# Kernel optimization log

Measured on AMD Instinct MI355X. Metric: run time of the kernel, lower is better.

The kernel has to match this reference:

```python
import jax, jax.numpy as jnp
import numpy as np

N = 10000      # nodes
E = 100000     # edges
D = 64         # node_out_feats
EH = 128       # edge_hidden_feats
NI = 74        # node_in_feats
EI = 12        # edge_in_feats
STEPS = 6


def _lin_init(key, fan_in, fan_out):
    s = 1.0 / np.sqrt(fan_in)
    kw, kb = jax.random.split(key)
    W = jax.random.uniform(kw, (fan_out, fan_in), minval=-s, maxval=s, dtype=jnp.float32)
    b = jax.random.uniform(kb, (fan_out,), minval=-s, maxval=s, dtype=jnp.float32)
    return W, b


def setup_inputs() -> dict:
    key = jax.random.key(0)
    ks = jax.random.split(key, 10)
    x = jax.random.normal(ks[0], (N, NI), dtype=jnp.float32)
    edge_index = jax.random.randint(ks[1], (2, E), 0, N, dtype=jnp.int64)
    edge_attr = jax.random.normal(ks[2], (E, EI), dtype=jnp.float32)
    W_proj, b_proj = _lin_init(ks[3], NI, D)
    W_e1, b_e1 = _lin_init(ks[4], EI, EH)
    W_e2, b_e2 = _lin_init(ks[5], EH, D * D)
    W_lin, b_lin = _lin_init(ks[6], D, D)
    s = 1.0 / np.sqrt(D)
    W_ih = jax.random.uniform(ks[7], (3 * D, D), minval=-s, maxval=s, dtype=jnp.float32)
    W_hh = jax.random.uniform(ks[8], (3 * D, D), minval=-s, maxval=s, dtype=jnp.float32)
    kb1, kb2 = jax.random.split(ks[9])
    b_ih = jax.random.uniform(kb1, (3 * D,), minval=-s, maxval=s, dtype=jnp.float32)
    b_hh = jax.random.uniform(kb2, (3 * D,), minval=-s, maxval=s, dtype=jnp.float32)
    return {"x": x, "edge_index": edge_index, "edge_attr": edge_attr,
            "W_proj": W_proj, "b_proj": b_proj,
            "W_e1": W_e1, "b_e1": b_e1, "W_e2": W_e2, "b_e2": b_e2,
            "W_lin": W_lin, "b_lin": b_lin,
            "W_ih": W_ih, "W_hh": W_hh, "b_ih": b_ih, "b_hh": b_hh}


def _gru_cell(x, h, W_ih, W_hh, b_ih, b_hh):
    # torch GRU gate layout: rows [r; z; n]
    gi = x @ W_ih.T + b_ih
    gh = h @ W_hh.T + b_hh
    i_r, i_z, i_n = jnp.split(gi, 3, axis=-1)
    h_r, h_z, h_n = jnp.split(gh, 3, axis=-1)
    r = jax.nn.sigmoid(i_r + h_r)
    z = jax.nn.sigmoid(i_z + h_z)
    n = jnp.tanh(i_n + r * h_n)
    return (1.0 - z) * n + z * h


def reference(x, edge_index, edge_attr, W_proj, b_proj, W_e1, b_e1, W_e2, b_e2,
              W_lin, b_lin, W_ih, W_hh, b_ih, b_hh):
    src = edge_index[0]
    dst = edge_index[1]
    n_nodes = x.shape[0]
    d = W_lin.shape[0]

    # project_node_feats
    node_feats = jax.nn.relu(x @ W_proj.T + b_proj)          # [N, D]
    hidden = node_feats                                       # h0 (never updated, per source)

    # edge network (identical each step in original; compute once)
    eh = jax.nn.relu(edge_attr @ W_e1.T + b_e1)               # [E, EH]
    A = (eh @ W_e2.T + b_e2).reshape(-1, d, d)                # [E, D, D]

    cnt = jax.ops.segment_sum(jnp.ones(src.shape, x.dtype), dst, num_segments=n_nodes)
    cnt = jnp.maximum(cnt, 1.0)[:, None]                      # mean divisor, 0-deg -> keep 0

    for _ in range(STEPS):
        xp = node_feats @ W_lin.T + b_lin                     # lin_node, [N, D]
        msg = jnp.einsum('ed,edf->ef', xp[src], A)            # per-edge bmm, [E, D]
        agg = jax.ops.segment_sum(msg, dst, num_segments=n_nodes) / cnt  # scatter-mean
        nf = jax.nn.relu(agg)
        node_feats = _gru_cell(nf, hidden, W_ih, W_hh, b_ih, b_hh)
    return node_feats
```

## Files before the change

### kernel.cpp

```cpp
#include <hip/hip_runtime.h>
#include <hip/hip_bf16.h>

#define NN 10000
#define NE 100000
#define DD 64
#define EH_ 128
#define NI_ 74
#define EI_ 12
#define NSTEPS 6
#define PADN 10240
#define GCAP 16384
#define EPB 64

#define RZ_OFF 0
#define NI_OFF 16384
#define NH_OFF 20480
#define WL_OFF 24576
#define BE_OFF 28672
#define G_TOT  32768

typedef short bf16x8 __attribute__((ext_vector_type(8)));
typedef float f32x4 __attribute__((ext_vector_type(4)));

static __device__ __forceinline__ unsigned short f2b(float f) {
    unsigned int u = __float_as_uint(f);
    u += 0x7fffu + ((u >> 16) & 1u);
    return (unsigned short)(u >> 16);
}

__global__ void k_zero(float* p, int n) {
    int i = blockIdx.x * blockDim.x + threadIdx.x;
    if (i < n) p[i] = 0.f;
}

__global__ void k_zero2(float* a, float* b, int n) {
    int i = blockIdx.x * blockDim.x + threadIdx.x;
    if (i < n) { a[i] = 0.f; b[i] = 0.f; }
}

__global__ void k_proj(const float* __restrict__ x, const float* __restrict__ Wp,
                       const float* __restrict__ bp, float* __restrict__ nf,
                       float* __restrict__ hid, unsigned short* __restrict__ hidb) {
    int w = (blockIdx.x * blockDim.x + threadIdx.x) >> 6;
    int lane = threadIdx.x & 63;
    if (w >= PADN) return;
    if (w >= NN) { hidb[(size_t)w * DD + lane] = 0; return; }
    const float* xr = x + (size_t)w * NI_;
    float x0 = xr[lane];
    float x1 = (lane < NI_ - 64) ? xr[64 + lane] : 0.f;
    float acc = bp[lane];
    const float* wr = Wp + (size_t)lane * NI_;
    #pragma unroll
    for (int i = 0; i < 64; i++) acc += __shfl(x0, i, 64) * wr[i];
    #pragma unroll
    for (int i = 0; i < NI_ - 64; i++) acc += __shfl(x1, i, 64) * wr[64 + i];
    acc = fmaxf(acc, 0.f);
    nf[(size_t)w * DD + lane] = acc;
    hid[(size_t)w * DD + lane] = acc;
    hidb[(size_t)w * DD + lane] = f2b(acc);
}

__global__ void k_degs(const int* __restrict__ srcv, const int* __restrict__ dstv,
                       int* __restrict__ hist, float* __restrict__ cnt) {
    int e = blockIdx.x * blockDim.x + threadIdx.x;
    if (e < NE) {
        atomicAdd(&hist[srcv[e]], 1);
        atomicAdd(&cnt[dstv[e]], 1.0f);
    }
}

__global__ void k_scangrp(const int* __restrict__ hist, int* __restrict__ rowptr,
                          int* __restrict__ cursor, int* __restrict__ g_src,
                          int* __restrict__ g_base, int* __restrict__ g_cnt,
                          int* __restrict__ d_ng) {
    __shared__ int part[1024];
    int t = threadIdx.x;
    const int PER = (NN + 1023) / 1024;
    int b0 = t * PER;
    int sum = 0;
    for (int i = 0; i < PER; i++) { int b = b0 + i; if (b < NN) sum += hist[b]; }
    part[t] = sum;
    __syncthreads();
    for (int off = 1; off < 1024; off <<= 1) {
        int v = (t >= off) ? part[t - off] : 0;
        __syncthreads();
        part[t] += v;
        __syncthreads();
    }
    int run = (t > 0) ? part[t - 1] : 0;
    for (int i = 0; i <= PER; i++) {
        int b = b0 + i;
        if (b <= NN) {
            rowptr[b] = run;
            if (b < NN) cursor[b] = run;
        }
        if (b < NN && i < PER) run += hist[b];
        if (i == PER) break;
    }
    __syncthreads();
    int cg = 0;
    for (int i = 0; i < PER; i++) {
        int b = b0 + i;
        if (b < NN) cg += (hist[b] + 15) >> 4;
    }
    part[t] = cg;
    __syncthreads();
    for (int off = 1; off < 1024; off <<= 1) {
        int v = (t >= off) ? part[t - off] : 0;
        __syncthreads();
        part[t] += v;
        __syncthreads();
    }
    int grun = (t > 0) ? part[t - 1] : 0;
    for (int i = 0; i < PER; i++) {
        int b = b0 + i;
        if (b >= NN) break;
        int r0 = rowptr[b], r1 = rowptr[b + 1];
        for (int p = r0; p < r1; p += 16) {
            g_src[grun] = b;
            g_base[grun] = p;
            int c = r1 - p; if (c > 16) c = 16;
            g_cnt[grun] = c;
            grun++;
        }
    }
    if (t == 1023) *d_ng = grun;
}

__global__ void k_scatter(const int* __restrict__ srcv, const int* __restrict__ dstv,
                          int* __restrict__ cursor, int* __restrict__ perm,
                          int* __restrict__ dsts_s) {
    int e = blockIdx.x * blockDim.x + threadIdx.x;
    if (e >= NE) return;
    int s = srcv[e];
    int pos = atomicAdd(&cursor[s], 1);
    perm[pos] = e;
    dsts_s[pos] = dstv[e];
}

__global__ void k_eh_s(const float* __restrict__ ea, const float* __restrict__ W1,
                       const float* __restrict__ b1, const int* __restrict__ perm,
                       unsigned short* __restrict__ ehs) {
    __shared__ float s_W[EH_ * EI_];
    __shared__ float s_b[EH_];
    __shared__ float s_ea[EPB][EI_];
    __shared__ int s_perm[EPB];
    int t = threadIdx.x;
    int p0 = blockIdx.x * EPB;
    for (int i = t; i < EH_ * EI_; i += 256) s_W[i] = W1[i];
    if (t < EH_) s_b[t] = b1[t];
    if (t < EPB) s_perm[t] = (p0 + t < NE) ? perm[p0 + t] : 0;
    __syncthreads();
    for (int i = t; i < EPB * EI_; i += 256) {
        int pl = i / EI_, ii = i % EI_;
        s_ea[pl][ii] = (p0 + pl < NE) ? ea[(size_t)s_perm[pl] * EI_ + ii] : 0.f;
    }
    int le = t >> 7;
    int h = t & 127;
    float wrow[EI_];
    #pragma unroll
    for (int i = 0; i < EI_; i++) wrow[i] = s_W[h * EI_ + i];
    float bb = s_b[h];
    __syncthreads();
    for (int pl = le; pl < EPB; pl += 2) {
        int p = p0 + pl;
        if (p >= NE) break;
        float acc = bb;
        #pragma unroll
        for (int i = 0; i < EI_; i++) acc += s_ea[pl][i] * wrow[i];
        ehs[(size_t)p * EH_ + h] = f2b(fmaxf(acc, 0.f));
    }
}

__global__ void k_pA(const float* __restrict__ W2, unsigned short* __restrict__ Apk) {
    int idx = blockIdx.x * 256 + threadIdx.x;
    if (idx >= (1 << 19)) return;
    int j = idx & 7;
    int n = (idx >> 3) & 15;
    int g = (idx >> 7) & 3;
    int frag = (idx >> 9) & 1;
    int f = (idx >> 10) & 63;
    int hB = (idx >> 16) & 1;
    int ks = idx >> 17;
    int d = frag * 32 + g * 8 + j;
    int h = ks * 32 + hB * 16 + n;
    Apk[idx] = f2b(W2[((size_t)(d * 64 + f)) * EH_ + h]);
}

__global__ void k_pG(const float* __restrict__ Wih, const float* __restrict__ Whh,
                     const float* __restrict__ Wl, const float* __restrict__ be2,
                     unsigned short* __restrict__ Gpk) {
    int idx = blockIdx.x * 256 + threadIdx.x;
    if (idx >= G_TOT) return;
    int j = idx & 7, n = (idx >> 3) & 15, g = (idx >> 7) & 3;
    float v;
    if (idx < NI_OFF) {
        int rem = idx >> 9;
        int q = rem & 3, ct = rem >> 2;
        int c = ct * 16 + n, k = q * 32 + g * 8 + j;
        v = (k < 64) ? Wih[(size_t)c * 64 + k] : Whh[(size_t)c * 64 + (k - 64)];
    } else if (idx < NH_OFF) {
        int l = idx - NI_OFF; int rem = l >> 9;
        int q = rem & 1, ct = rem >> 1;
        int c = ct * 16 + n, k = q * 32 + g * 8 + j;
        v = Wih[(size_t)(128 + c) * 64 + k];
    } else if (idx < WL_OFF) {
        int l = idx - NH_OFF; int rem = l >> 9;
        int q = rem & 1, ct = rem >> 1;
        int c = ct * 16 + n, k = q * 32 + g * 8 + j;
        v = Whh[(size_t)(128 + c) * 64 + k];
    } else if (idx < BE_OFF) {
        int l = idx - WL_OFF; int rem = l >> 9;
        int q = rem & 1, ct = rem >> 1;
        int c = ct * 16 + n, k = q * 32 + g * 8 + j;
        v = Wl[(size_t)c * 64 + k];
    } else {
        int l = idx - BE_OFF; int rem = l >> 9;
        int q = rem & 1, ct = rem >> 1;
        int c = ct * 16 + n, k = q * 32 + g * 8 + j;
        v = be2[(size_t)k * 64 + c];
    }
    Gpk[idx] = f2b(v);
}

__global__ void k_tr64(const float* __restrict__ W, float* __restrict__ Wt) {
    int idx = blockIdx.x * 256 + threadIdx.x;
    if (idx >= 64 * 64) return;
    int r = idx >> 6, c = idx & 63;
    Wt[c * 64 + r] = W[idx];
}

__global__ void k_prep(const float* __restrict__ agg, const float* __restrict__ cnt,
                       unsigned short* __restrict__ nfvb, float* aggw) {
    int i = blockIdx.x * 256 + threadIdx.x;
    if (i >= PADN * DD) return;
    int node = i >> 6;
    if (node >= NN) { nfvb[i] = 0; return; }
    float c = fmaxf(cnt[node], 1.f);
    nfvb[i] = f2b(fmaxf(agg[i] / c, 0.f));
    aggw[i] = 0.f;
}

__global__ void k_xp(const float* __restrict__ nf, const float* __restrict__ WlT,
                     const float* __restrict__ bl, const float* __restrict__ be2,
                     unsigned short* __restrict__ xpb, float* __restrict__ btp,
                     float* __restrict__ agg) {
    int wid = (blockIdx.x * blockDim.x + threadIdx.x) >> 6;
    int lane = threadIdx.x & 63;
    int s0 = wid * 4;
    if (s0 >= NN) return;
    int nv = (NN - s0 < 4) ? (NN - s0) : 4;
    float nvv[4], acc[4], bt[4];
    float blv = bl[lane];
    #pragma unroll
    for (int i = 0; i < 4; i++) {
        int s = s0 + (i < nv ? i : nv - 1);
        nvv[i] = nf[(size_t)s * DD + lane];
        acc[i] = blv;
        bt[i] = 0.f;
    }
    for (int d = 0; d < 64; d++) {
        float wv = WlT[d * 64 + lane];
        #pragma unroll
        for (int i = 0; i < 4; i++)
            acc[i] = fmaf(__shfl(nvv[i], d, 64), wv, acc[i]);
    }
    for (int d = 0; d < 64; d++) {
        float bv = be2[d * 64 + lane];
        #pragma unroll
        for (int i = 0; i < 4; i++)
            bt[i] = fmaf(__shfl(acc[i], d, 64), bv, bt[i]);
    }
    #pragma unroll
    for (int i = 0; i < 4; i++) {
        if (i < nv) {
            xpb[(size_t)(s0 + i) * DD + lane] = f2b(acc[i]);
            btp[(size_t)(s0 + i) * DD + lane] = bt[i];
            agg[(size_t)(s0 + i) * DD + lane] = 0.f;
        }
    }
}

__global__ __launch_bounds__(1024, 8) void k_fv(
        const unsigned short* __restrict__ xpb,
        const unsigned short* __restrict__ Apk,
        const int* __restrict__ g_src, const int* __restrict__ g_base,
        const int* __restrict__ g_cnt, const int* __restrict__ d_ng,
        const unsigned short* __restrict__ ehs, const int* __restrict__ dsts,
        const float* __restrict__ btp, float* __restrict__ agg) {
    __shared__ unsigned char lds[65536];
    int ng = *d_ng;
    int nb = blockIdx.x * 16;
    if (nb >= ng) return;
    int tid = threadIdx.x;
    int w = tid >> 6, lane = tid & 63;
    int g = lane >> 4, n = lane & 15;

    int srcn = g_src[nb + n];
    const unsigned short* xr = xpb + (size_t)srcn * DD + g * 8;
    bf16x8 xb0 = *(const bf16x8*)xr;
    bf16x8 xb1 = *(const bf16x8*)(xr + 32);

    int gi = nb + w;
    int sq = g_src[gi], bq = g_base[gi], cq = g_cnt[gi];

    f32x4 acc[4];
    #pragma unroll
    for (int nt = 0; nt < 4; nt++) {
        f32x4 z = {0.f, 0.f, 0.f, 0.f};
        acc[nt] = z;
    }

    for (int ks = 0; ks < 4; ks++) {
        if (ks) __syncthreads();
        #pragma unroll
        for (int hB = 0; hB < 2; hB++) {
            int ho = hB * 2 + (g >> 1);
            int hq0 = (g & 1) * 4;
            int abase = (n << 12) | (ho << 4) | (hq0 << 1);
            const unsigned short* apks =
                Apk + (size_t)((ks * 2 + hB) * 64 + (w << 2)) * 1024 + g * 128 + n * 8;
            #pragma unroll
            for (int fi = 0; fi < 4; fi++) {
                int f = (w << 2) + fi;
                const unsigned short* ap = apks + fi * 1024;
                bf16x8 A0 = *(const bf16x8*)ap;
                bf16x8 A1 = *(const bf16x8*)(ap + 512);
                f32x4 d = {0.f, 0.f, 0.f, 0.f};
                d = __builtin_amdgcn_mfma_f32_16x16x32_bf16(A0, xb0, d, 0, 0, 0);
                d = __builtin_amdgcn_mfma_f32_16x16x32_bf16(A1, xb1, d, 0, 0, 0);
                unsigned int lo = (unsigned)f2b(d[0]) | ((unsigned)f2b(d[1]) << 16);
                unsigned int hi = (unsigned)f2b(d[2]) | ((unsigned)f2b(d[3]) << 16);
                int addr = abase | (f << 6);
                addr ^= ((n ^ f) & 7) << 4;
                *(unsigned long long*)(lds + addr) =
                    (unsigned long long)lo | ((unsigned long long)hi << 32);
            }
        }
        bf16x8 aeh = *(const bf16x8*)(ehs + (size_t)(bq + n) * EH_ + ks * 32 + g * 8);
        __syncthreads();
        bf16x8 Bf[4];
        #pragma unroll
        for (int nt = 0; nt < 4; nt++) {
            int f = nt * 16 + n;
            int addr = (w << 12) | (f << 6) | (g << 4);
            addr ^= ((w ^ f) & 7) << 4;
            Bf[nt] = *(const bf16x8*)(lds + addr);
        }
        #pragma unroll
        for (int nt = 0; nt < 4; nt++)
            acc[nt] = __builtin_amdgcn_mfma_f32_16x16x32_bf16(aeh, Bf[nt], acc[nt], 0, 0, 0);
    }
    if (cq == 0) return;
    #pragma unroll
    for (int nt = 0; nt < 4; nt++) {
        float btv = btp[(size_t)sq * DD + nt * 16 + n];
        #pragma unroll
        for (int rg = 0; rg < 4; rg++) {
            int m = g * 4 + rg;
            if (m < cq) {
                int dn = dsts[bq + m];
                atomicAdd(&agg[(size_t)dn * DD + nt * 16 + n], acc[nt][rg] + btv);
            }
        }
    }
}

__global__ void k_gx(const unsigned short* __restrict__ nfvb,
                     const unsigned short* __restrict__ hidb,
                     const float* __restrict__ hid,
                     const unsigned short* __restrict__ Gpk,
                     const float* __restrict__ bih, const float* __restrict__ bhh,
                     const float* __restrict__ bl,
                     float* __restrict__ out_nf, unsigned short* __restrict__ xpb,
                     float* __restrict__ btp, int doXp) {
    __shared__ unsigned short s_nf[64 * 64];
    __shared__ unsigned short s_xp[64 * 64];
    int tid = threadIdx.x;
    int w = tid >> 6, lane = tid & 63;
    int g = lane >> 4, n = lane & 15;
    int nb = blockIdx.x * 64;
    int jj = w * 16 + n;

    bf16x8 Br[4], Bz[4], Bi[2], Bh[2], Bw[2], Be[2];
    #pragma unroll
    for (int q = 0; q < 4; q++) {
        Br[q] = *(const bf16x8*)(Gpk + RZ_OFF + (size_t)(((w) * 4 + q) * 4 + g) * 128 + n * 8);
        Bz[q] = *(const bf16x8*)(Gpk + RZ_OFF + (size_t)(((w + 4) * 4 + q) * 4 + g) * 128 + n * 8);
    }
    #pragma unroll
    for (int q = 0; q < 2; q++) {
        Bi[q] = *(const bf16x8*)(Gpk + NI_OFF + (size_t)((w * 2 + q) * 4 + g) * 128 + n * 8);
        Bh[q] = *(const bf16x8*)(Gpk + NH_OFF + (size_t)((w * 2 + q) * 4 + g) * 128 + n * 8);
        Bw[q] = *(const bf16x8*)(Gpk + WL_OFF + (size_t)((w * 2 + q) * 4 + g) * 128 + n * 8);
        Be[q] = *(const bf16x8*)(Gpk + BE_OFF + (size_t)((w * 2 + q) * 4 + g) * 128 + n * 8);
    }
    float br_ = bih[jj] + bhh[jj];
    float bz_ = bih[64 + jj] + bhh[64 + jj];
    float bi_ = bih[128 + jj];
    float bh_ = bhh[128 + jj];
    float blv = bl[jj];

    #pragma unroll
    for (int mt = 0; mt < 4; mt++) {
        int arow = nb + mt * 16 + n;
        const unsigned short* na = nfvb + (size_t)arow * DD + g * 8;
        const unsigned short* ha = hidb + (size_t)arow * DD + g * 8;
        bf16x8 A0 = *(const bf16x8*)na, A1 = *(const bf16x8*)(na + 32);
        bf16x8 H0 = *(const bf16x8*)ha, H1 = *(const bf16x8*)(ha + 32);
        f32x4 aR = {0.f, 0.f, 0.f, 0.f}, aZ = aR, aI = aR, aH = aR;
        aR = __builtin_amdgcn_mfma_f32_16x16x32_bf16(A0, Br[0], aR, 0, 0, 0);
        aR = __builtin_amdgcn_mfma_f32_16x16x32_bf16(A1, Br[1], aR, 0, 0, 0);
        aR = __builtin_amdgcn_mfma_f32_16x16x32_bf16(H0, Br[2], aR, 0, 0, 0);
        aR = __builtin_amdgcn_mfma_f32_16x16x32_bf16(H1, Br[3], aR, 0, 0, 0);
        aZ = __builtin_amdgcn_mfma_f32_16x16x32_bf16(A0, Bz[0], aZ, 0, 0, 0);
        aZ = __builtin_amdgcn_mfma_f32_16x16x32_bf16(A1, Bz[1], aZ, 0, 0, 0);
        aZ = __builtin_amdgcn_mfma_f32_16x16x32_bf16(H0, Bz[2], aZ, 0, 0, 0);
        aZ = __builtin_amdgcn_mfma_f32_16x16x32_bf16(H1, Bz[3], aZ, 0, 0, 0);
        aI = __builtin_amdgcn_mfma_f32_16x16x32_bf16(A0, Bi[0], aI, 0, 0, 0);
        aI = __builtin_amdgcn_mfma_f32_16x16x32_bf16(A1, Bi[1], aI, 0, 0, 0);
        aH = __builtin_amdgcn_mfma_f32_16x16x32_bf16(H0, Bh[0], aH, 0, 0, 0);
        aH = __builtin_amdgcn_mfma_f32_16x16x32_bf16(H1, Bh[1], aH, 0, 0, 0);
        #pragma unroll
        for (int rg = 0; rg < 4; rg++) {
            int row = mt * 16 + g * 4 + rg;
            int node = nb + row;
            float r = 1.f / (1.f + __expf(-(aR[rg] + br_)));
            float z = 1.f / (1.f + __expf(-(aZ[rg] + bz_)));
            float nn2 = tanhf(aI[rg] + bi_ + r * (aH[rg] + bh_));
            float hv = (node < NN) ? hid[(size_t)node * DD + jj] : 0.f;
            float nf_ = (1.f - z) * nn2 + z * hv;
            if (node < NN) out_nf[(size_t)node * DD + jj] = nf_;
            int ba = (row * 128 + jj * 2) ^ ((row & 7) << 4);
            s_nf[ba >> 1] = f2b(nf_);
        }
    }
    if (!doXp) return;
    __syncthreads();
    #pragma unroll
    for (int mt = 0; mt < 4; mt++) {
        int row = mt * 16 + n;
        int sw = (row & 7) << 4;
        bf16x8 X0 = *(const bf16x8*)((const unsigned char*)s_nf + ((row * 128 + g * 16) ^ sw));
        bf16x8 X1 = *(const bf16x8*)((const unsigned char*)s_nf + ((row * 128 + 64 + g * 16) ^ sw));
        f32x4 aX = {0.f, 0.f, 0.f, 0.f};
        aX = __builtin_amdgcn_mfma_f32_16x16x32_bf16(X0, Bw[0], aX, 0, 0, 0);
        aX = __builtin_amdgcn_mfma_f32_16x16x32_bf16(X1, Bw[1], aX, 0, 0, 0);
        #pragma unroll
        for (int rg = 0; rg < 4; rg++) {
            int row2 = mt * 16 + g * 4 + rg;
            int ba = (row2 * 128 + jj * 2) ^ ((row2 & 7) << 4);
            s_xp[ba >> 1] = f2b(aX[rg] + blv);
        }
    }
    __syncthreads();
    {
        int row = w * 16 + n;
        int sw = (row & 7) << 4;
        #pragma unroll
        for (int h2 = 0; h2 < 2; h2++) {
            int byteo = (row * 128 + (h2 * 4 + g) * 16) ^ sw;
            bf16x8 v = *(const bf16x8*)((const unsigned char*)s_xp + byteo);
            *(bf16x8*)(xpb + (size_t)(nb + row) * DD + (h2 * 4 + g) * 8) = v;
        }
    }
    #pragma unroll
    for (int mt = 0; mt < 4; mt++) {
        int row = mt * 16 + n;
        int sw = (row & 7) << 4;
        bf16x8 X0 = *(const bf16x8*)((const unsigned char*)s_xp + ((row * 128 + g * 16) ^ sw));
        bf16x8 X1 = *(const bf16x8*)((const unsigned char*)s_xp + ((row * 128 + 64 + g * 16) ^ sw));
        f32x4 aB = {0.f, 0.f, 0.f, 0.f};
        aB = __builtin_amdgcn_mfma_f32_16x16x32_bf16(X0, Be[0], aB, 0, 0, 0);
        aB = __builtin_amdgcn_mfma_f32_16x16x32_bf16(X1, Be[1], aB, 0, 0, 0);
        #pragma unroll
        for (int rg = 0; rg < 4; rg++) {
            int node = nb + mt * 16 + g * 4 + rg;
            if (node < NN) btp[(size_t)node * DD + jj] = aB[rg];
        }
    }
}

extern "C" void kernel_launch(void* const* d_in, const int* in_sizes, int n_in,
                              void* d_out, int out_size, void* d_ws, size_t ws_size,
                              hipStream_t stream) {
    const float* x   = (const float*)d_in[0];
    const int*   ei  = (const int*)d_in[1];
    const float* ea  = (const float*)d_in[2];
    const float* Wp  = (const float*)d_in[3];
    const float* bp  = (const float*)d_in[4];
    const float* W1  = (const float*)d_in[5];
    const float* b1  = (const float*)d_in[6];
    const float* W2  = (const float*)d_in[7];
    const float* b2  = (const float*)d_in[8];
    const float* Wl  = (const float*)d_in[9];
    const float* bl  = (const float*)d_in[10];
    const float* Wih = (const float*)d_in[11];
    const float* Whh = (const float*)d_in[12];
    const float* bih = (const float*)d_in[13];
    const float* bhh = (const float*)d_in[14];
    const int* srcv = ei;
    const int* dstv = ei + NE;

    float* p = (float*)d_ws;
    size_t off = 0;
    auto alloc = [&](size_t n) { n = (n + 3) & ~(size_t)3; float* q = p + off; off += n; return q; };
    float* nf   = alloc((size_t)NN * DD);
    float* hid  = alloc((size_t)NN * DD);
    float* btp  = alloc((size_t)NN * DD);
    float* agg  = alloc((size_t)NN * DD);
    float* cnt  = alloc(NN);
    unsigned short* ehs = (unsigned short*)alloc((size_t)(NE + 16) * EH_ / 2);
    float* WlT  = alloc(64 * 64);
    int* hist   = (int*)alloc(NN);
    int* rowptr = (int*)alloc(NN + 1);
    int* cursor = (int*)alloc(NN);
    int* perm   = (int*)alloc(NE);
    int* dsts_s = (int*)alloc(NE);
    int* g_src  = (int*)alloc(GCAP);
    int* g_base = (int*)alloc(GCAP);
    int* g_cnt  = (int*)alloc(GCAP);
    int* d_ng   = (int*)alloc(4);
    unsigned short* Apk  = (unsigned short*)alloc((size_t)(1 << 19) / 2);
    unsigned short* Gpk  = (unsigned short*)alloc((size_t)G_TOT / 2);
    unsigned short* xpb  = (unsigned short*)alloc((size_t)PADN * DD / 2);
    unsigned short* nfvb = (unsigned short*)alloc((size_t)PADN * DD / 2);
    unsigned short* hidb = (unsigned short*)alloc((size_t)PADN * DD / 2);

    k_zero2<<<(NN + 255) / 256, 256, 0, stream>>>(cnt, (float*)hist, NN);
    k_zero<<<(3 * GCAP + 255) / 256, 256, 0, stream>>>((float*)g_src, 3 * GCAP);
    k_proj<<<(PADN + 3) / 4, 256, 0, stream>>>(x, Wp, bp, nf, hid, hidb);
    k_pA<<<(1 << 19) / 256, 256, 0, stream>>>(W2, Apk);
    k_pG<<<(G_TOT + 255) / 256, 256, 0, stream>>>(Wih, Whh, Wl, b2, Gpk);
    k_tr64<<<16, 256, 0, stream>>>(Wl, WlT);
    k_degs<<<(NE + 255) / 256, 256, 0, stream>>>(srcv, dstv, hist, cnt);
    k_scangrp<<<1, 1024, 0, stream>>>(hist, rowptr, cursor, g_src, g_base, g_cnt, d_ng);
    k_scatter<<<(NE + 255) / 256, 256, 0, stream>>>(srcv, dstv, cursor, perm, dsts_s);
    k_eh_s<<<(NE + EPB - 1) / EPB, 256, 0, stream>>>(ea, W1, b1, perm, ehs);

    const int nw_quarter = (NN + 3) / 4;
    const int gx_blocks = (NN + 63) / 64;
    k_xp<<<(nw_quarter + 3) / 4, 256, 0, stream>>>(nf, WlT, bl, b2, xpb, btp, agg);
    for (int s = 0; s < NSTEPS; s++) {
        k_fv<<<GCAP / 16, 1024, 0, stream>>>(xpb, Apk, g_src, g_base, g_cnt, d_ng,
                                             ehs, dsts_s, btp, agg);
        k_prep<<<(PADN * DD + 255) / 256, 256, 0, stream>>>(agg, cnt, nfvb, agg);
        float* dest = (s == NSTEPS - 1) ? (float*)d_out : nf;
        k_gx<<<gx_blocks, 256, 0, stream>>>(nfvb, hidb, hid, Gpk, bih, bhh, bl,
                                            dest, xpb, btp,
                                            (s < NSTEPS - 1) ? 1 : 0);
    }
}
```

Baseline: 555.0 us.

## Replace atomic scatter-add with per-edge messages and CSR gather by destination

```diff
diff --git a/kernel.cpp b/kernel.cpp
--- a/kernel.cpp
+++ b/kernel.cpp
@@ -61,18 +61,19 @@
 }
 
 __global__ void k_degs(const int* __restrict__ srcv, const int* __restrict__ dstv,
-                       int* __restrict__ hist, float* __restrict__ cnt) {
+                       int* __restrict__ hist, int* __restrict__ histd) {
     int e = blockIdx.x * blockDim.x + threadIdx.x;
     if (e < NE) {
         atomicAdd(&hist[srcv[e]], 1);
-        atomicAdd(&cnt[dstv[e]], 1.0f);
-    }
-}
-
-__global__ void k_scangrp(const int* __restrict__ hist, int* __restrict__ rowptr,
-                          int* __restrict__ cursor, int* __restrict__ g_src,
-                          int* __restrict__ g_base, int* __restrict__ g_cnt,
-                          int* __restrict__ d_ng) {
+        atomicAdd(&histd[dstv[e]], 1);
+    }
+}
+
+__global__ void k_scangrp(const int* __restrict__ hist, const int* __restrict__ histd,
+                          int* __restrict__ rowptr, int* __restrict__ cursor,
+                          int* __restrict__ g_src, int* __restrict__ g_base,
+                          int* __restrict__ g_cnt, int* __restrict__ d_ng,
+                          int* __restrict__ rowptrd, int* __restrict__ cursord) {
     __shared__ int part[1024];
     int t = threadIdx.x;
     const int PER = (NN + 1023) / 1024;
@@ -125,17 +126,40 @@
         }
     }
     if (t == 1023) *d_ng = grun;
+    __syncthreads();
+    int sumd = 0;
+    for (int i = 0; i < PER; i++) { int b = b0 + i; if (b < NN) sumd += histd[b]; }
+    part[t] = sumd;
+    __syncthreads();
+    for (int off = 1; off < 1024; off <<= 1) {
+        int v = (t >= off) ? part[t - off] : 0;
+        __syncthreads();
+        part[t] += v;
+        __syncthreads();
+    }
+    int rund = (t > 0) ? part[t - 1] : 0;
+    for (int i = 0; i <= PER; i++) {
+        int b = b0 + i;
+        if (b <= NN) {
+            rowptrd[b] = rund;
+            if (b < NN) cursord[b] = rund;
+        }
+        if (b < NN && i < PER) rund += histd[b];
+        if (i == PER) break;
+    }
 }
 
 __global__ void k_scatter(const int* __restrict__ srcv, const int* __restrict__ dstv,
-                          int* __restrict__ cursor, int* __restrict__ perm,
-                          int* __restrict__ dsts_s) {
+                          int* __restrict__ cursor, int* __restrict__ cursord,
+                          int* __restrict__ perm, int* __restrict__ permd) {
     int e = blockIdx.x * blockDim.x + threadIdx.x;
     if (e >= NE) return;
     int s = srcv[e];
+    int d = dstv[e];
     int pos = atomicAdd(&cursor[s], 1);
     perm[pos] = e;
-    dsts_s[pos] = dstv[e];
+    int posd = atomicAdd(&cursord[d], 1);
+    permd[posd] = pos;
 }
 
 __global__ void k_eh_s(const float* __restrict__ ea, const float* __restrict__ W1,
@@ -230,21 +254,31 @@
     Wt[c * 64 + r] = W[idx];
 }
 
-__global__ void k_prep(const float* __restrict__ agg, const float* __restrict__ cnt,
-                       unsigned short* __restrict__ nfvb, float* aggw) {
-    int i = blockIdx.x * 256 + threadIdx.x;
-    if (i >= PADN * DD) return;
-    int node = i >> 6;
-    if (node >= NN) { nfvb[i] = 0; return; }
-    float c = fmaxf(cnt[node], 1.f);
-    nfvb[i] = f2b(fmaxf(agg[i] / c, 0.f));
-    aggw[i] = 0.f;
+__global__ void k_prep(const float* __restrict__ msg, const int* __restrict__ rowptrd,
+                       const int* __restrict__ permd, unsigned short* __restrict__ nfvb) {
+    int wid = (blockIdx.x * blockDim.x + threadIdx.x) >> 6;
+    int lane = threadIdx.x & 63;
+    int s0 = wid * 4;
+    if (s0 >= PADN) return;
+    #pragma unroll
+    for (int i = 0; i < 4; i++) {
+        int node = s0 + i;
+        if (node >= PADN) break;
+        if (node >= NN) { nfvb[(size_t)node * DD + lane] = 0; continue; }
+        int r0 = rowptrd[node], r1 = rowptrd[node + 1];
+        float acc = 0.f;
+        for (int p = r0; p < r1; p++) {
+            int sp = permd[p];
+            acc += msg[(size_t)sp * DD + lane];
+        }
+        float c = fmaxf((float)(r1 - r0), 1.f);
+        nfvb[(size_t)node * DD + lane] = f2b(fmaxf(acc / c, 0.f));
+    }
 }
 
 __global__ void k_xp(const float* __restrict__ nf, const float* __restrict__ WlT,
                      const float* __restrict__ bl, const float* __restrict__ be2,
-                     unsigned short* __restrict__ xpb, float* __restrict__ btp,
-                     float* __restrict__ agg) {
+                     unsigned short* __restrict__ xpb, float* __restrict__ btp) {
     int wid = (blockIdx.x * blockDim.x + threadIdx.x) >> 6;
     int lane = threadIdx.x & 63;
     int s0 = wid * 4;
@@ -276,7 +310,6 @@
         if (i < nv) {
             xpb[(size_t)(s0 + i) * DD + lane] = f2b(acc[i]);
             btp[(size_t)(s0 + i) * DD + lane] = bt[i];
-            agg[(size_t)(s0 + i) * DD + lane] = 0.f;
         }
     }
 }
@@ -286,8 +319,8 @@
         const unsigned short* __restrict__ Apk,
         const int* __restrict__ g_src, const int* __restrict__ g_base,
         const int* __restrict__ g_cnt, const int* __restrict__ d_ng,
-        const unsigned short* __restrict__ ehs, const int* __restrict__ dsts,
-        const float* __restrict__ btp, float* __restrict__ agg) {
+        const unsigned short* __restrict__ ehs,
+        const float* __restrict__ btp, float* __restrict__ msg) {
     __shared__ unsigned char lds[65536];
     int ng = *d_ng;
     int nb = blockIdx.x * 16;
@@ -358,10 +391,8 @@
         #pragma unroll
         for (int rg = 0; rg < 4; rg++) {
             int m = g * 4 + rg;
-            if (m < cq) {
-                int dn = dsts[bq + m];
-                atomicAdd(&agg[(size_t)dn * DD + nt * 16 + n], acc[nt][rg] + btv);
-            }
+            if (m < cq)
+                msg[(size_t)(bq + m) * DD + nt * 16 + n] = acc[nt][rg] + btv;
         }
     }
 }
@@ -508,15 +539,16 @@
     float* nf   = alloc((size_t)NN * DD);
     float* hid  = alloc((size_t)NN * DD);
     float* btp  = alloc((size_t)NN * DD);
-    float* agg  = alloc((size_t)NN * DD);
-    float* cnt  = alloc(NN);
     unsigned short* ehs = (unsigned short*)alloc((size_t)(NE + 16) * EH_ / 2);
     float* WlT  = alloc(64 * 64);
     int* hist   = (int*)alloc(NN);
+    int* histd  = (int*)alloc(NN);
     int* rowptr = (int*)alloc(NN + 1);
     int* cursor = (int*)alloc(NN);
+    int* rowptrd = (int*)alloc(NN + 1);
+    int* cursord = (int*)alloc(NN);
     int* perm   = (int*)alloc(NE);
-    int* dsts_s = (int*)alloc(NE);
+    int* permd  = (int*)alloc(NE);
     int* g_src  = (int*)alloc(GCAP);
     int* g_base = (int*)alloc(GCAP);
     int* g_cnt  = (int*)alloc(GCAP);
@@ -526,25 +558,29 @@
     unsigned short* xpb  = (unsigned short*)alloc((size_t)PADN * DD / 2);
     unsigned short* nfvb = (unsigned short*)alloc((size_t)PADN * DD / 2);
     unsigned short* hidb = (unsigned short*)alloc((size_t)PADN * DD / 2);
-
-    k_zero2<<<(NN + 255) / 256, 256, 0, stream>>>(cnt, (float*)hist, NN);
+    float* msg = alloc((size_t)NE * DD);
+
+    k_zero<<<(2 * NN + 255) / 256, 256, 0, stream>>>((float*)hist, 2 * NN);
     k_zero<<<(3 * GCAP + 255) / 256, 256, 0, stream>>>((float*)g_src, 3 * GCAP);
     k_proj<<<(PADN + 3) / 4, 256, 0, stream>>>(x, Wp, bp, nf, hid, hidb);
     k_pA<<<(1 << 19) / 256, 256, 0, stream>>>(W2, Apk);
     k_pG<<<(G_TOT + 255) / 256, 256, 0, stream>>>(Wih, Whh, Wl, b2, Gpk);
     k_tr64<<<16, 256, 0, stream>>>(Wl, WlT);
-    k_degs<<<(NE + 255) / 256, 256, 0, stream>>>(srcv, dstv, hist, cnt);
-    k_scangrp<<<1, 1024, 0, stream>>>(hist, rowptr, cursor, g_src, g_base, g_cnt, d_ng);
-    k_scatter<<<(NE + 255) / 256, 256, 0, stream>>>(srcv, dstv, cursor, perm, dsts_s);
+    k_degs<<<(NE + 255) / 256, 256, 0, stream>>>(srcv, dstv, hist, histd);
+    k_scangrp<<<1, 1024, 0, stream>>>(hist, histd, rowptr, cursor,
+                                      g_src, g_base, g_cnt, d_ng, rowptrd, cursord);
+    k_scatter<<<(NE + 255) / 256, 256, 0, stream>>>(srcv, dstv, cursor, cursord,
+                                                    perm, permd);
     k_eh_s<<<(NE + EPB - 1) / EPB, 256, 0, stream>>>(ea, W1, b1, perm, ehs);
 
     const int nw_quarter = (NN + 3) / 4;
     const int gx_blocks = (NN + 63) / 64;
-    k_xp<<<(nw_quarter + 3) / 4, 256, 0, stream>>>(nf, WlT, bl, b2, xpb, btp, agg);
+    const int prep_blocks = (PADN / 4 + 3) / 4;
+    k_xp<<<(nw_quarter + 3) / 4, 256, 0, stream>>>(nf, WlT, bl, b2, xpb, btp);
     for (int s = 0; s < NSTEPS; s++) {
         k_fv<<<GCAP / 16, 1024, 0, stream>>>(xpb, Apk, g_src, g_base, g_cnt, d_ng,
-                                             ehs, dsts_s, btp, agg);
-        k_prep<<<(PADN * DD + 255) / 256, 256, 0, stream>>>(agg, cnt, nfvb, agg);
+                                             ehs, btp, msg);
+        k_prep<<<prep_blocks, 256, 0, stream>>>(msg, rowptrd, permd, nfvb);
         float* dest = (s == NSTEPS - 1) ? (float*)d_out : nf;
         k_gx<<<gx_blocks, 256, 0, stream>>>(nfvb, hidb, hid, Gpk, bih, bhh, bl,
                                             dest, xpb, btp,
```

Measured after the change: 676.4 us. 1.22x slower.
